# Performance work log

Measured on AMD Instinct MI355X. Metric: run time of the kernel, lower is better.

## Reference

```python
import jax, jax.numpy as jnp
import numpy as np

D_MODEL = 1024
NUM_HEADS = 16


def setup_inputs() -> dict:
    key = jax.random.key(0)
    ks = jax.random.split(key, 5)
    std = float(np.sqrt(2.0 / (D_MODEL + D_MODEL)))
    def w(k):
        # approximate trunc_normal init with clipped normal (init only; math of fwd unaffected)
        v = jax.random.truncated_normal(k, -3.0, 3.0, (D_MODEL, D_MODEL), jnp.float32) * std
        return v
    x = jax.random.normal(ks[0], (4, 2048, D_MODEL), jnp.float32)
    return {
        "x": x,
        "wq": w(ks[1]),
        "wk": w(ks[2]),
        "wv": w(ks[3]),
        "wo": w(ks[4]),
    }


def reference(x, wq, wk, wv, wo):
    b, s, d = x.shape
    h = NUM_HEADS
    dk = d // h
    # Linear: einsum('o i, ... i -> ... o')
    def proj(w):
        y = jnp.einsum('oi,bsi->bso', w, x)
        return y.reshape(b, s, h, dk).transpose(0, 2, 1, 3)  # b h s dk
    Q, K, V = proj(wq), proj(wk), proj(wv)
    scale = 1.0 / jnp.sqrt(jnp.asarray(dk, x.dtype))
    scores = jnp.einsum('bhqd,bhkd->bhqk', Q, K) * scale
    mask = jnp.tril(jnp.ones((s, s), dtype=bool))
    scores = jnp.where(mask, scores, -jnp.inf)
    attn = jax.nn.softmax(scores, axis=-1)
    out = jnp.einsum('bhqk,bhkd->bhqd', attn, V)
    out = out.transpose(0, 2, 1, 3).reshape(b, s, d)
    return jnp.einsum('oi,bsi->bso', wo, out)
```

## Files before the change

kernel.cpp:

```cpp
#include <hip/hip_runtime.h>
#include <hip/hip_bf16.h>


typedef __bf16 bf16x8 __attribute__((ext_vector_type(8)));
typedef __bf16 bf16x4 __attribute__((ext_vector_type(4)));
typedef float  f32x4  __attribute__((ext_vector_type(4)));
typedef float  f32x16 __attribute__((ext_vector_type(16)));
typedef unsigned int u32x4_t __attribute__((ext_vector_type(4)));

#define GLOBAL_AS __attribute__((address_space(1)))
#define LDS_AS    __attribute__((address_space(3)))

__device__ __forceinline__ void gload16(const void* g, void* l) {
    __builtin_amdgcn_global_load_lds((const GLOBAL_AS void*)g, (LDS_AS void*)l, 16, 0, 0);
}

__device__ __forceinline__ unsigned int cvtpk_bf16(float lo, float hi) {
    unsigned int r;
    asm("v_cvt_pk_bf16_f32 %0, %1, %2" : "=v"(r) : "v"(lo), "v"(hi));
    return r;
}

#define WAITVM8 asm volatile("s_waitcnt vmcnt(8)" ::: "memory")
#define WAITVM6 asm volatile("s_waitcnt vmcnt(6)" ::: "memory")
#define WAITVM0 asm volatile("s_waitcnt vmcnt(0)" ::: "memory")
#define SCHEDB  __builtin_amdgcn_sched_barrier(0)

__global__ __launch_bounds__(256) void cast_kernel(
    const float* __restrict__ x, const float* __restrict__ wq,
    const float* __restrict__ wk, const float* __restrict__ wv,
    const float* __restrict__ wo, __bf16* __restrict__ xb, __bf16* __restrict__ wb) {
    int bid = blockIdx.x;
    const float* src; __bf16* dst; int base;
    if (bid < 4096) {
        src = x; dst = xb; base = bid * 2048;
    } else {
        int r = bid - 4096; int wi = r >> 9;
        src = (wi == 0) ? wq : (wi == 1) ? wk : (wi == 2) ? wv : wo;
        dst = wb + wi * 1048576; base = (r & 511) * 2048;
    }
    int idx = base + threadIdx.x * 8;
    float4 a = *(const float4*)(src + idx);
    float4 b = *(const float4*)(src + idx + 4);
    bf16x8 o;
    o[0] = (__bf16)a.x; o[1] = (__bf16)a.y; o[2] = (__bf16)a.z; o[3] = (__bf16)a.w;
    o[4] = (__bf16)b.x; o[5] = (__bf16)b.y; o[6] = (__bf16)b.z; o[7] = (__bf16)b.w;
    *(bf16x8*)(dst + idx) = o;
}

__global__ __launch_bounds__(512, 2) void gemm_qkv_kernel(
    const __bf16* __restrict__ A, const __bf16* __restrict__ W,
    __bf16* __restrict__ Qb, __bf16* __restrict__ Kb, __bf16* __restrict__ Vt,
    float qscale) {
    __shared__ __align__(16) char lds[147456];
    const int t = threadIdx.x;
    const int wid = t >> 6, lane = t & 63;
    const int g = lane >> 4, m = lane & 15;
    const int wm = wid >> 2, wn = wid & 3;
    const int bid = (blockIdx.x & 7) * 96 + (blockIdx.x >> 3);
    const int mt = bid / 12, nt = bid % 12;
    const int m0 = mt * 128, n0 = nt * 256;
    const bool isV = (n0 >= 2048);

    const __bf16* sA[2]; int dA[2];
#pragma unroll
    for (int i = 0; i < 2; ++i) {
        const int ci = i * 512 + t;
        const int row = ci >> 3;
        const int k8 = (ci & 7) ^ (row & 7);
        sA[i] = A + (size_t)(m0 + row) * 1024 + k8 * 8;
        dA[i] = ci * 16;
    }
    const __bf16* sB[4]; int dB[4];
#pragma unroll
    for (int i = 0; i < 4; ++i) {
        const int ci = i * 512 + t;
        const int row = ci >> 3;
        const int k8 = (ci & 7) ^ (row & 7);
        sB[i] = W + (size_t)(n0 + row) * 1024 + k8 * 8;
        dB[i] = ci * 16;
    }
    auto stage = [&](int kt, char* buf) {
        gload16(sA[0] + kt * 64, buf + dA[0]);
        gload16(sA[1] + kt * 64, buf + dA[1]);
        gload16(sB[0] + kt * 64, buf + 16384 + dB[0]);
        gload16(sB[1] + kt * 64, buf + 16384 + dB[1]);
        gload16(sB[2] + kt * 64, buf + 16384 + dB[2]);
        gload16(sB[3] + kt * 64, buf + 16384 + dB[3]);
    };

    const int sw = (m & 7) << 4;
    const int offA = (wm * 64 + m) * 128 + ((g << 4) ^ sw);
    const int offB = (wn * 64 + m) * 128 + ((g << 4) ^ sw);

    stage(0, lds);
    stage(1, lds + 49152);
    WAITVM6;
    SCHEDB;
    __builtin_amdgcn_s_barrier();
    SCHEDB;

    f32x4 acc[4][4] = {};
    for (int kt = 0; kt < 16; ++kt) {
        char* cbuf = lds + (kt % 3) * 49152;
        if (kt < 14) stage(kt + 2, lds + ((kt + 2) % 3) * 49152);
        const char* bA = cbuf;
        const char* bB = cbuf + 16384;
        bf16x8 a0[4], b0[4], a1[4], b1[4];
#pragma unroll
        for (int i = 0; i < 4; ++i) {
            a0[i] = *(const bf16x8*)(bA + (offA + i * 2048));
            b0[i] = *(const bf16x8*)(bB + (offB + i * 2048));
            a1[i] = *(const bf16x8*)(bA + ((offA + i * 2048) ^ 64));
            b1[i] = *(const bf16x8*)(bB + ((offB + i * 2048) ^ 64));
        }
        __builtin_amdgcn_s_setprio(1);
        if (isV) {
#pragma unroll
            for (int mi = 0; mi < 4; ++mi)
#pragma unroll
                for (int ni = 0; ni < 4; ++ni)
                    acc[mi][ni] = __builtin_amdgcn_mfma_f32_16x16x32_bf16(a0[mi], b0[ni], acc[mi][ni], 0, 0, 0);
#pragma unroll
            for (int mi = 0; mi < 4; ++mi)
#pragma unroll
                for (int ni = 0; ni < 4; ++ni)
                    acc[mi][ni] = __builtin_amdgcn_mfma_f32_16x16x32_bf16(a1[mi], b1[ni], acc[mi][ni], 0, 0, 0);
        } else {
#pragma unroll
            for (int mi = 0; mi < 4; ++mi)
#pragma unroll
                for (int ni = 0; ni < 4; ++ni)
                    acc[mi][ni] = __builtin_amdgcn_mfma_f32_16x16x32_bf16(b0[ni], a0[mi], acc[mi][ni], 0, 0, 0);
#pragma unroll
            for (int mi = 0; mi < 4; ++mi)
#pragma unroll
                for (int ni = 0; ni < 4; ++ni)
                    acc[mi][ni] = __builtin_amdgcn_mfma_f32_16x16x32_bf16(b1[ni], a1[mi], acc[mi][ni], 0, 0, 0);
        }
        __builtin_amdgcn_s_setprio(0);
        if (kt < 14) { WAITVM6; }
        else if (kt == 14) { WAITVM0; }
        if (kt < 15) {
            SCHEDB;
            __builtin_amdgcn_s_barrier();
            SCHEDB;
        }
    }

    if (isV) {
        const int bb = m0 >> 11;
        const int sb = (m0 & 2047) + wm * 64 + 4 * g;
        const int hbase = ((n0 - 2048) >> 6) + wn;
#pragma unroll
        for (int mi = 0; mi < 4; ++mi)
#pragma unroll
            for (int ni = 0; ni < 4; ++ni) {
                const int d = ni * 16 + m;
                bf16x4 pk;
                pk[0] = (__bf16)(acc[mi][ni][0]); pk[1] = (__bf16)(acc[mi][ni][1]);
                pk[2] = (__bf16)(acc[mi][ni][2]); pk[3] = (__bf16)(acc[mi][ni][3]);
                *(bf16x4*)(Vt + ((size_t)(bb * 16 + hbase) * 64 + d) * 2048 + sb + mi * 16) = pk;
            }
    } else {
        __bf16* C = (n0 < 1024) ? Qb : Kb;
        const float sc = (n0 < 1024) ? qscale : 1.f;
        const int cb = (n0 & 1023) + wn * 64 + 4 * g;
        const int row = m0 + wm * 64 + m;
#pragma unroll
        for (int mi = 0; mi < 4; ++mi)
#pragma unroll
            for (int ni = 0; ni < 4; ++ni) {
                bf16x4 pk;
                pk[0] = (__bf16)(acc[mi][ni][0] * sc); pk[1] = (__bf16)(acc[mi][ni][1] * sc);
                pk[2] = (__bf16)(acc[mi][ni][2] * sc); pk[3] = (__bf16)(acc[mi][ni][3] * sc);
                *(bf16x4*)(C + (size_t)(row + mi * 16) * 1024 + cb + ni * 16) = pk;
            }
    }
}

__global__ __launch_bounds__(512, 2) void gemm_out_kernel(
    const __bf16* __restrict__ A, const __bf16* __restrict__ W, float* __restrict__ out) {
    __shared__ __align__(16) char lds[147456];
    const int t = threadIdx.x;
    const int wid = t >> 6, lane = t & 63;
    const int g = lane >> 4, m = lane & 15;
    const int wm = wid >> 2, wn = wid & 3;
    const int bid = (blockIdx.x & 7) * 32 + (blockIdx.x >> 3);
    const int mt = bid >> 2, nt = bid & 3;
    const int m0 = mt * 128, n0 = nt * 256;

    const __bf16* sA[2]; int dA[2];
#pragma unroll
    for (int i = 0; i < 2; ++i) {
        const int ci = i * 512 + t;
        const int row = ci >> 3;
        const int k8 = (ci & 7) ^ (row & 7);
        sA[i] = A + (size_t)(m0 + row) * 1024 + k8 * 8;
        dA[i] = ci * 16;
    }
    const __bf16* sB[4]; int dB[4];
#pragma unroll
    for (int i = 0; i < 4; ++i) {
        const int ci = i * 512 + t;
        const int row = ci >> 3;
        const int k8 = (ci & 7) ^ (row & 7);
        sB[i] = W + (size_t)(n0 + row) * 1024 + k8 * 8;
        dB[i] = ci * 16;
    }
    auto stage = [&](int kt, char* buf) {
        gload16(sA[0] + kt * 64, buf + dA[0]);
        gload16(sA[1] + kt * 64, buf + dA[1]);
        gload16(sB[0] + kt * 64, buf + 16384 + dB[0]);
        gload16(sB[1] + kt * 64, buf + 16384 + dB[1]);
        gload16(sB[2] + kt * 64, buf + 16384 + dB[2]);
        gload16(sB[3] + kt * 64, buf + 16384 + dB[3]);
    };

    const int sw = (m & 7) << 4;
    const int offA = (wm * 64 + m) * 128 + ((g << 4) ^ sw);
    const int offB = (wn * 64 + m) * 128 + ((g << 4) ^ sw);

    stage(0, lds);
    stage(1, lds + 49152);
    WAITVM6;
    SCHEDB;
    __builtin_amdgcn_s_barrier();
    SCHEDB;

    f32x4 acc[4][4] = {};
    for (int kt = 0; kt < 16; ++kt) {
        char* cbuf = lds + (kt % 3) * 49152;
        if (kt < 14) stage(kt + 2, lds + ((kt + 2) % 3) * 49152);
        const char* bA = cbuf;
        const char* bB = cbuf + 16384;
        bf16x8 a0[4], b0[4], a1[4], b1[4];
#pragma unroll
        for (int i = 0; i < 4; ++i) {
            a0[i] = *(const bf16x8*)(bA + (offA + i * 2048));
            b0[i] = *(const bf16x8*)(bB + (offB + i * 2048));
            a1[i] = *(const bf16x8*)(bA + ((offA + i * 2048) ^ 64));
            b1[i] = *(const bf16x8*)(bB + ((offB + i * 2048) ^ 64));
        }
        __builtin_amdgcn_s_setprio(1);
#pragma unroll
        for (int mi = 0; mi < 4; ++mi)
#pragma unroll
            for (int ni = 0; ni < 4; ++ni)
                acc[mi][ni] = __builtin_amdgcn_mfma_f32_16x16x32_bf16(b0[ni], a0[mi], acc[mi][ni], 0, 0, 0);
#pragma unroll
        for (int mi = 0; mi < 4; ++mi)
#pragma unroll
            for (int ni = 0; ni < 4; ++ni)
                acc[mi][ni] = __builtin_amdgcn_mfma_f32_16x16x32_bf16(b1[ni], a1[mi], acc[mi][ni], 0, 0, 0);
        __builtin_amdgcn_s_setprio(0);
        if (kt < 14) { WAITVM6; }
        else if (kt == 14) { WAITVM0; }
        if (kt < 15) {
            SCHEDB;
            __builtin_amdgcn_s_barrier();
            SCHEDB;
        }
    }

    const int row = m0 + wm * 64 + m;
    const int col = n0 + wn * 64 + 4 * g;
#pragma unroll
    for (int mi = 0; mi < 4; ++mi)
#pragma unroll
        for (int ni = 0; ni < 4; ++ni)
            *(f32x4*)(out + (size_t)(row + mi * 16) * 1024 + col + ni * 16) = acc[mi][ni];
}

__global__ __launch_bounds__(128, 2) void attn_kernel(
    const __bf16* __restrict__ Qb, const __bf16* __restrict__ Kb,
    const __bf16* __restrict__ Vt, __bf16* __restrict__ Ob) {
    __shared__ __align__(16) char lds[32768];
    const int t = threadIdx.x;
    const int w = t >> 6, lane = t & 63;
    const int l31 = lane & 31, hi = lane >> 5;
    const int qb = (blockIdx.x >> 3) & 15;
    const int bh = (blockIdx.x & 7) | ((blockIdx.x >> 7) << 3);
    const size_t sbase = (size_t)(bh >> 4) * 2048;
    const int hoff = (bh & 15) * 64;

    const char* Kbase = (const char*)Kb + (sbase * 1024 + hoff) * 2;
    const char* Vbase = (const char*)Vt + (size_t)bh * 262144;
    const int srow = lane >> 3;
    const int scol = ((lane & 7) ^ srow) << 4;
    const int sw = (l31 & 7) << 4;
    int colx[4];
#pragma unroll
    for (int i = 0; i < 4; ++i) colx[i] = (32 * i + 16 * hi) ^ sw;

    auto stage = [&](int kv0, char* lK) {
        char* lV = lK + 8192;
#pragma unroll
        for (int i = 0; i < 4; ++i) {
            const int chunk = i * 2 + w;
            const int row = chunk * 8 + srow;
            gload16(Kbase + (size_t)(kv0 + row) * 2048 + scol, lK + chunk * 1024);
            gload16(Vbase + (size_t)row * 4096 + (size_t)kv0 * 2 + scol, lV + chunk * 1024);
        }
    };

    const int q0A = qb * 64 + w * 32;
    const int q0B = (31 - qb) * 64 + w * 32;
    const int qA = q0A + l31, qB = q0B + l31;
    const int nstream = 32 - qb;

    const __bf16* qrowA = Qb + (sbase + q0A + l31) * 1024 + hoff + 8 * hi;
    const __bf16* qrowB = Qb + (sbase + q0B + l31) * 1024 + hoff + 8 * hi;
    bf16x8 qfA[4], qfB[4];
#pragma unroll
    for (int cq = 0; cq < 4; ++cq) {
        qfA[cq] = *(const bf16x8*)(qrowA + 16 * cq);
        qfB[cq] = *(const bf16x8*)(qrowB + 16 * cq);
    }

    f32x16 oA0 = {}, oA1 = {}, oB0 = {}, oB1 = {};
    float mA = -__builtin_inff(), lA = 0.f;
    float mB = -__builtin_inff(), lB = 0.f;

    auto process = [&](const f32x16& s0r, const f32x16& s1r, int qq, bool diag,
                       int kv0, float& mrun, float& lrun, f32x16& o0, f32x16& o1,
                       const char* lV) {
        float pp[32];
#pragma unroll
        for (int rr = 0; rr < 16; ++rr) { pp[rr] = s0r[rr]; pp[16 + rr] = s1r[rr]; }
        if (diag) {
#pragma unroll
            for (int rr = 0; rr < 16; ++rr) {
                const int kvl = (rr & 3) + 8 * (rr >> 2) + 4 * hi;
                if (kv0 + kvl > qq)      pp[rr]      = -__builtin_inff();
                if (kv0 + 32 + kvl > qq) pp[16 + rr] = -__builtin_inff();
            }
        }
        float m8[8];
#pragma unroll
        for (int i = 0; i < 8; ++i)
            m8[i] = fmaxf(fmaxf(pp[4 * i], pp[4 * i + 1]), fmaxf(pp[4 * i + 2], pp[4 * i + 3]));
        float tmax = fmaxf(fmaxf(fmaxf(m8[0], m8[1]), fmaxf(m8[2], m8[3])),
                           fmaxf(fmaxf(m8[4], m8[5]), fmaxf(m8[6], m8[7])));
        const bool skip = __all(tmax <= mrun + 8.f);
        if (!skip) {
            float tq = fmaxf(tmax, __shfl_xor(tmax, 32));
            float mnew = fmaxf(mrun, tq);
            float al = __builtin_amdgcn_exp2f(mrun - mnew);
            lrun *= al;
#pragma unroll
            for (int rr = 0; rr < 16; ++rr) { o0[rr] *= al; o1[rr] *= al; }
            mrun = mnew;
        }
#pragma unroll
        for (int rr = 0; rr < 32; ++rr) pp[rr] = __builtin_amdgcn_exp2f(pp[rr] - mrun);
        float s8[8];
#pragma unroll
        for (int i = 0; i < 8; ++i)
            s8[i] = (pp[4 * i] + pp[4 * i + 1]) + (pp[4 * i + 2] + pp[4 * i + 3]);
        float rsum = ((s8[0] + s8[1]) + (s8[2] + s8[3])) + ((s8[4] + s8[5]) + (s8[6] + s8[7]));
        rsum += __shfl_xor(rsum, 32);
        lrun += rsum;

        __builtin_amdgcn_s_setprio(1);
#pragma unroll
        for (int cc = 0; cc < 4; ++cc) {
            const int pb = cc * 8;
            unsigned int A0 = cvtpk_bf16(pp[pb + 0], pp[pb + 1]);
            unsigned int A1 = cvtpk_bf16(pp[pb + 2], pp[pb + 3]);
            unsigned int B0 = cvtpk_bf16(pp[pb + 4], pp[pb + 5]);
            unsigned int B1 = cvtpk_bf16(pp[pb + 6], pp[pb + 7]);
            asm("v_permlane32_swap_b32 %0, %1" : "+v"(A0), "+v"(B0));
            asm("v_permlane32_swap_b32 %0, %1" : "+v"(A1), "+v"(B1));
            u32x4_t wvv; wvv[0] = A0; wvv[1] = A1; wvv[2] = B0; wvv[3] = B1;
            bf16x8 pa = __builtin_bit_cast(bf16x8, wvv);
            const int vcol = (32 * cc + 16 * hi) ^ sw;
            bf16x8 v0 = *(const bf16x8*)(lV + l31 * 128 + vcol);
            bf16x8 v1 = *(const bf16x8*)(lV + (l31 + 32) * 128 + vcol);
            o0 = __builtin_amdgcn_mfma_f32_32x32x16_bf16(v0, pa, o0, 0, 0, 0);
            o1 = __builtin_amdgcn_mfma_f32_32x32x16_bf16(v1, pa, o1, 0, 0, 0);
        }
        __builtin_amdgcn_s_setprio(0);
    };

    stage(0, lds);

    for (int tt = 0; tt < nstream; ++tt) {
        const int cur = tt & 1;
        char* lcur = lds + cur * 16384;
        __builtin_amdgcn_s_barrier();
        if (tt + 1 < nstream) {
            stage((tt + 1) * 64, lds + (cur ^ 1) * 16384);
            WAITVM8;
        } else {
            WAITVM0;
        }
        __builtin_amdgcn_s_barrier();
        __builtin_amdgcn_sched_barrier(0);

        const int kv0 = tt * 64;
        const char* lK = lcur;
        const char* lV = lcur + 8192;
        const bool dual = (tt <= qb);

        f32x16 sA0 = {}, sA1 = {}, sB0 = {}, sB1 = {};
        __builtin_amdgcn_s_setprio(1);
        if (dual) {
#pragma unroll
            for (int cc = 0; cc < 4; ++cc) {
                bf16x8 k0 = *(const bf16x8*)(lK + l31 * 128 + colx[cc]);
                bf16x8 k1 = *(const bf16x8*)(lK + (l31 + 32) * 128 + colx[cc]);
                sA0 = __builtin_amdgcn_mfma_f32_32x32x16_bf16(k0, qfA[cc], sA0, 0, 0, 0);
                sA1 = __builtin_amdgcn_mfma_f32_32x32x16_bf16(k1, qfA[cc], sA1, 0, 0, 0);
                sB0 = __builtin_amdgcn_mfma_f32_32x32x16_bf16(k0, qfB[cc], sB0, 0, 0, 0);
                sB1 = __builtin_amdgcn_mfma_f32_32x32x16_bf16(k1, qfB[cc], sB1, 0, 0, 0);
            }
        } else {
#pragma unroll
            for (int cc = 0; cc < 4; ++cc) {
                bf16x8 k0 = *(const bf16x8*)(lK + l31 * 128 + colx[cc]);
                bf16x8 k1 = *(const bf16x8*)(lK + (l31 + 32) * 128 + colx[cc]);
                sB0 = __builtin_amdgcn_mfma_f32_32x32x16_bf16(k0, qfB[cc], sB0, 0, 0, 0);
                sB1 = __builtin_amdgcn_mfma_f32_32x32x16_bf16(k1, qfB[cc], sB1, 0, 0, 0);
            }
        }
        __builtin_amdgcn_s_setprio(0);

        if (dual)
            process(sA0, sA1, qA, tt == qb, kv0, mA, lA, oA0, oA1, lV);
        process(sB0, sB1, qB, tt == nstream - 1, kv0, mB, lB, oB0, oB1, lV);
    }

    {
        const float inv = 1.f / lA;
        __bf16* orow = Ob + (sbase + q0A + l31) * 1024 + hoff;
#pragma unroll
        for (int rq = 0; rq < 4; ++rq) {
            bf16x4 e0, e1;
#pragma unroll
            for (int jj = 0; jj < 4; ++jj) {
                e0[jj] = (__bf16)(oA0[rq * 4 + jj] * inv);
                e1[jj] = (__bf16)(oA1[rq * 4 + jj] * inv);
            }
            *(bf16x4*)(orow + 4 * hi + 8 * rq) = e0;
            *(bf16x4*)(orow + 32 + 4 * hi + 8 * rq) = e1;
        }
    }
    {
        const float inv = 1.f / lB;
        __bf16* orow = Ob + (sbase + q0B + l31) * 1024 + hoff;
#pragma unroll
        for (int rq = 0; rq < 4; ++rq) {
            bf16x4 e0, e1;
#pragma unroll
            for (int jj = 0; jj < 4; ++jj) {
                e0[jj] = (__bf16)(oB0[rq * 4 + jj] * inv);
                e1[jj] = (__bf16)(oB1[rq * 4 + jj] * inv);
            }
            *(bf16x4*)(orow + 4 * hi + 8 * rq) = e0;
            *(bf16x4*)(orow + 32 + 4 * hi + 8 * rq) = e1;
        }
    }
}

extern "C" void kernel_launch(void* const* d_in, const int* in_sizes, int n_in,
                              void* d_out, int out_size, void* d_ws, size_t ws_size,
                              hipStream_t stream) {
    const float* x  = (const float*)d_in[0];
    const float* wq = (const float*)d_in[1];
    const float* wk = (const float*)d_in[2];
    const float* wv = (const float*)d_in[3];
    const float* wo = (const float*)d_in[4];

    char* ws = (char*)d_ws;
    __bf16* xb = (__bf16*)(ws);
    __bf16* wb = (__bf16*)(ws + 16777216);
    __bf16* Qb = (__bf16*)(ws + 25165824);
    __bf16* Kb = (__bf16*)(ws + 41943040);
    __bf16* Vt = (__bf16*)(ws + 58720256);
    __bf16* Ob = (__bf16*)(ws + 75497472);

    const float qscale = 0.18033688011112043f;

    cast_kernel<<<6144, 256, 0, stream>>>(x, wq, wk, wv, wo, xb, wb);
    gemm_qkv_kernel<<<768, 512, 0, stream>>>(xb, wb, Qb, Kb, Vt, qscale);
    attn_kernel<<<1024, 128, 0, stream>>>(Qb, Kb, Vt, Ob);
    gemm_out_kernel<<<256, 512, 0, stream>>>(Ob, wb + 3145728, (float*)d_out);
}
```

Measured before the change: 180.9 us.

## Shrink GEMM tiles to 128x128 with 4 waves and double-buffered LDS

Both projection GEMMs move from 128x256 tiles with 8 waves and a 3-stage LDS ring to 128x128 tiles with 4 waves and a 2-stage ring, doubling the grid. Each block stages 8 loads per k-step and waits for the current stage after issuing the next. The aim is more blocks per CU and better wave balance (512 blocks instead of 256 for the output GEMM). In exchange each tile does less reuse per byte loaded, and prefetch depth drops from two stages to one, exposing more load latency.

```diff
diff --git a/kernel.cpp b/kernel.cpp
--- a/kernel.cpp
+++ b/kernel.cpp
@@ -22,7 +22,6 @@
 }
 
 #define WAITVM8 asm volatile("s_waitcnt vmcnt(8)" ::: "memory")
-#define WAITVM6 asm volatile("s_waitcnt vmcnt(6)" ::: "memory")
 #define WAITVM0 asm volatile("s_waitcnt vmcnt(0)" ::: "memory")
 #define SCHEDB  __builtin_amdgcn_sched_barrier(0)
 
@@ -48,45 +47,35 @@
     *(bf16x8*)(dst + idx) = o;
 }
 
-__global__ __launch_bounds__(512, 2) void gemm_qkv_kernel(
+__global__ __launch_bounds__(256) void gemm_qkv_kernel(
     const __bf16* __restrict__ A, const __bf16* __restrict__ W,
     __bf16* __restrict__ Qb, __bf16* __restrict__ Kb, __bf16* __restrict__ Vt,
     float qscale) {
-    __shared__ __align__(16) char lds[147456];
+    __shared__ __align__(16) char lds[65536];
     const int t = threadIdx.x;
     const int wid = t >> 6, lane = t & 63;
     const int g = lane >> 4, m = lane & 15;
-    const int wm = wid >> 2, wn = wid & 3;
-    const int bid = (blockIdx.x & 7) * 96 + (blockIdx.x >> 3);
-    const int mt = bid / 12, nt = bid % 12;
-    const int m0 = mt * 128, n0 = nt * 256;
+    const int wm = wid >> 1, wn = wid & 1;
+    const int bid = (blockIdx.x & 7) * 192 + (blockIdx.x >> 3);
+    const int mt = bid / 24, nt = bid % 24;
+    const int m0 = mt * 128, n0 = nt * 128;
     const bool isV = (n0 >= 2048);
 
-    const __bf16* sA[2]; int dA[2];
-#pragma unroll
-    for (int i = 0; i < 2; ++i) {
-        const int ci = i * 512 + t;
+    const __bf16* sA[4]; const __bf16* sB[4]; int dA[4];
+#pragma unroll
+    for (int i = 0; i < 4; ++i) {
+        const int ci = i * 256 + t;
         const int row = ci >> 3;
         const int k8 = (ci & 7) ^ (row & 7);
         sA[i] = A + (size_t)(m0 + row) * 1024 + k8 * 8;
+        sB[i] = W + (size_t)(n0 + row) * 1024 + k8 * 8;
         dA[i] = ci * 16;
     }
-    const __bf16* sB[4]; int dB[4];
-#pragma unroll
-    for (int i = 0; i < 4; ++i) {
-        const int ci = i * 512 + t;
-        const int row = ci >> 3;
-        const int k8 = (ci & 7) ^ (row & 7);
-        sB[i] = W + (size_t)(n0 + row) * 1024 + k8 * 8;
-        dB[i] = ci * 16;
-    }
     auto stage = [&](int kt, char* buf) {
-        gload16(sA[0] + kt * 64, buf + dA[0]);
-        gload16(sA[1] + kt * 64, buf + dA[1]);
-        gload16(sB[0] + kt * 64, buf + 16384 + dB[0]);
-        gload16(sB[1] + kt * 64, buf + 16384 + dB[1]);
-        gload16(sB[2] + kt * 64, buf + 16384 + dB[2]);
-        gload16(sB[3] + kt * 64, buf + 16384 + dB[3]);
+#pragma unroll
+        for (int i = 0; i < 4; ++i) gload16(sA[i] + kt * 64, buf + dA[i]);
+#pragma unroll
+        for (int i = 0; i < 4; ++i) gload16(sB[i] + kt * 64, buf + 16384 + dA[i]);
     };
 
     const int sw = (m & 7) << 4;
@@ -94,16 +83,19 @@
     const int offB = (wn * 64 + m) * 128 + ((g << 4) ^ sw);
 
     stage(0, lds);
-    stage(1, lds + 49152);
-    WAITVM6;
-    SCHEDB;
-    __builtin_amdgcn_s_barrier();
-    SCHEDB;
 
     f32x4 acc[4][4] = {};
     for (int kt = 0; kt < 16; ++kt) {
-        char* cbuf = lds + (kt % 3) * 49152;
-        if (kt < 14) stage(kt + 2, lds + ((kt + 2) % 3) * 49152);
+        char* cbuf = lds + (kt & 1) * 32768;
+        if (kt < 15) {
+            stage(kt + 1, lds + ((kt + 1) & 1) * 32768);
+            WAITVM8;
+        } else {
+            WAITVM0;
+        }
+        SCHEDB;
+        __builtin_amdgcn_s_barrier();
+        SCHEDB;
         const char* bA = cbuf;
         const char* bB = cbuf + 16384;
         bf16x8 a0[4], b0[4], a1[4], b1[4];
@@ -139,8 +131,6 @@
                     acc[mi][ni] = __builtin_amdgcn_mfma_f32_16x16x32_bf16(b1[ni], a1[mi], acc[mi][ni], 0, 0, 0);
         }
         __builtin_amdgcn_s_setprio(0);
-        if (kt < 14) { WAITVM6; }
-        else if (kt == 14) { WAITVM0; }
         if (kt < 15) {
             SCHEDB;
             __builtin_amdgcn_s_barrier();
@@ -179,42 +169,32 @@
     }
 }
 
-__global__ __launch_bounds__(512, 2) void gemm_out_kernel(
+__global__ __launch_bounds__(256) void gemm_out_kernel(
     const __bf16* __restrict__ A, const __bf16* __restrict__ W, float* __restrict__ out) {
-    __shared__ __align__(16) char lds[147456];
+    __shared__ __align__(16) char lds[65536];
     const int t = threadIdx.x;
     const int wid = t >> 6, lane = t & 63;
     const int g = lane >> 4, m = lane & 15;
-    const int wm = wid >> 2, wn = wid & 3;
-    const int bid = (blockIdx.x & 7) * 32 + (blockIdx.x >> 3);
-    const int mt = bid >> 2, nt = bid & 3;
-    const int m0 = mt * 128, n0 = nt * 256;
-
-    const __bf16* sA[2]; int dA[2];
-#pragma unroll
-    for (int i = 0; i < 2; ++i) {
-        const int ci = i * 512 + t;
+    const int wm = wid >> 1, wn = wid & 1;
+    const int bid = (blockIdx.x & 7) * 64 + (blockIdx.x >> 3);
+    const int mt = bid >> 3, nt = bid & 7;
+    const int m0 = mt * 128, n0 = nt * 128;
+
+    const __bf16* sA[4]; const __bf16* sB[4]; int dA[4];
+#pragma unroll
+    for (int i = 0; i < 4; ++i) {
+        const int ci = i * 256 + t;
         const int row = ci >> 3;
         const int k8 = (ci & 7) ^ (row & 7);
         sA[i] = A + (size_t)(m0 + row) * 1024 + k8 * 8;
+        sB[i] = W + (size_t)(n0 + row) * 1024 + k8 * 8;
         dA[i] = ci * 16;
     }
-    const __bf16* sB[4]; int dB[4];
-#pragma unroll
-    for (int i = 0; i < 4; ++i) {
-        const int ci = i * 512 + t;
-        const int row = ci >> 3;
-        const int k8 = (ci & 7) ^ (row & 7);
-        sB[i] = W + (size_t)(n0 + row) * 1024 + k8 * 8;
-        dB[i] = ci * 16;
-    }
     auto stage = [&](int kt, char* buf) {
-        gload16(sA[0] + kt * 64, buf + dA[0]);
-        gload16(sA[1] + kt * 64, buf + dA[1]);
-        gload16(sB[0] + kt * 64, buf + 16384 + dB[0]);
-        gload16(sB[1] + kt * 64, buf + 16384 + dB[1]);
-        gload16(sB[2] + kt * 64, buf + 16384 + dB[2]);
-        gload16(sB[3] + kt * 64, buf + 16384 + dB[3]);
+#pragma unroll
+        for (int i = 0; i < 4; ++i) gload16(sA[i] + kt * 64, buf + dA[i]);
+#pragma unroll
+        for (int i = 0; i < 4; ++i) gload16(sB[i] + kt * 64, buf + 16384 + dA[i]);
     };
 
     const int sw = (m & 7) << 4;
@@ -222,16 +202,19 @@
     const int offB = (wn * 64 + m) * 128 + ((g << 4) ^ sw);
 
     stage(0, lds);
-    stage(1, lds + 49152);
-    WAITVM6;
-    SCHEDB;
-    __builtin_amdgcn_s_barrier();
-    SCHEDB;
 
     f32x4 acc[4][4] = {};
     for (int kt = 0; kt < 16; ++kt) {
-        char* cbuf = lds + (kt % 3) * 49152;
-        if (kt < 14) stage(kt + 2, lds + ((kt + 2) % 3) * 49152);
+        char* cbuf = lds + (kt & 1) * 32768;
+        if (kt < 15) {
+            stage(kt + 1, lds + ((kt + 1) & 1) * 32768);
+            WAITVM8;
+        } else {
+            WAITVM0;
+        }
+        SCHEDB;
+        __builtin_amdgcn_s_barrier();
+        SCHEDB;
         const char* bA = cbuf;
         const char* bB = cbuf + 16384;
         bf16x8 a0[4], b0[4], a1[4], b1[4];
@@ -254,8 +237,6 @@
             for (int ni = 0; ni < 4; ++ni)
                 acc[mi][ni] = __builtin_amdgcn_mfma_f32_16x16x32_bf16(b1[ni], a1[mi], acc[mi][ni], 0, 0, 0);
         __builtin_amdgcn_s_setprio(0);
-        if (kt < 14) { WAITVM6; }
-        else if (kt == 14) { WAITVM0; }
         if (kt < 15) {
             SCHEDB;
             __builtin_amdgcn_s_barrier();
@@ -483,7 +464,7 @@
     const float qscale = 0.18033688011112043f;
 
     cast_kernel<<<6144, 256, 0, stream>>>(x, wq, wk, wv, wo, xb, wb);
-    gemm_qkv_kernel<<<768, 512, 0, stream>>>(xb, wb, Qb, Kb, Vt, qscale);
+    gemm_qkv_kernel<<<1536, 256, 0, stream>>>(xb, wb, Qb, Kb, Vt, qscale);
     attn_kernel<<<1024, 128, 0, stream>>>(Qb, Kb, Vt, Ob);
-    gemm_out_kernel<<<256, 512, 0, stream>>>(Ob, wb + 3145728, (float*)d_out);
-}
+    gemm_out_kernel<<<512, 256, 0, stream>>>(Ob, wb + 3145728, (float*)d_out);
+}
```

Result: faster. 174.1 us (-3.8%).
